# Optimization experiments

Measured on AMD Instinct MI355X. Metric: run time of the kernel, lower is better.

The kernel has to match this reference:

```python
import jax, jax.numpy as jnp
import numpy as np

TEMPERATURE = 0.1


def setup_inputs() -> dict:
    key = jax.random.key(0)
    k1, k2 = jax.random.split(key)
    N, D = 8192, 128
    features = jax.random.normal(k1, (N, D), dtype=jnp.float32)
    labels = jax.random.randint(k2, (N,), 0, 1000, dtype=jnp.int64)
    return {"features": features, "labels": labels}


def reference(features, labels):
    N = features.shape[0]
    # L2-normalize rows
    feats = features / jnp.linalg.norm(features, axis=1, keepdims=True)
    # positive-pair mask from labels [N, N]
    labels = labels.reshape(-1, 1)
    mask = (labels == labels.T).astype(feats.dtype)
    # similarity matrix scaled by temperature
    sim = jnp.matmul(feats, feats.T) / TEMPERATURE
    # exclude self-comparisons (diagonal)
    logits_mask = 1.0 - jnp.eye(N, dtype=feats.dtype)
    mask = mask * logits_mask
    exp_logits = jnp.exp(sim) * logits_mask
    log_prob = sim - jnp.log(exp_logits.sum(axis=1, keepdims=True) + 1e-9)
    mask_sum = mask.sum(axis=1)
    mask_sum = jnp.where(mask_sum == 0, jnp.ones_like(mask_sum), mask_sum)
    mean_log_prob_pos = (mask * log_prob).sum(axis=1) / mask_sum
    return -mean_log_prob_pos.mean()
```

## Files before the change

kernel.cpp:

```cpp
#include <hip/hip_runtime.h>
#include <hip/hip_bf16.h>
#include <math.h>


constexpr int N = 8192;
constexpr int D = 128;

typedef __attribute__((ext_vector_type(8))) short short8;
typedef __attribute__((ext_vector_type(4))) float f32x4;

constexpr float SELF_POISON = -50.0f;

__device__ __forceinline__ float fast_exp2(float x) {
#if __has_builtin(__builtin_amdgcn_exp2f)
    return __builtin_amdgcn_exp2f(x);
#else
    return __expf(x * 0.69314718056f);
#endif
}

__global__ void zero_kernel(int* __restrict__ hist, float* __restrict__ out) {
    hist[threadIdx.x] = 0;
    if (threadIdx.x == 0) out[0] = 0.0f;
}

__global__ void prep_kernel(const float* __restrict__ F,
                            const int* __restrict__ labels,
                            unsigned int* __restrict__ FbP,
                            int* __restrict__ hist) {
    int row = blockIdx.x * 4 + (threadIdx.x >> 6);
    int l = threadIdx.x & 63;
    float2 v = ((const float2*)(F + (size_t)row * D))[l];
    float ss = v.x * v.x + v.y * v.y;
#pragma unroll
    for (int off = 32; off > 0; off >>= 1) ss += __shfl_xor(ss, off);
    float sc = sqrtf(14.4269504089f / ss);
    __hip_bfloat16 hx = __float2bfloat16(v.x * sc);
    __hip_bfloat16 hy = __float2bfloat16(v.y * sc);
    unsigned int ux = *(unsigned short*)&hx;
    unsigned int uy = *(unsigned short*)&hy;
    unsigned int idx = ((unsigned)(row >> 4) << 10) | ((unsigned)(l >> 2) << 6) |
                       ((unsigned)(row & 15) << 2) | (unsigned)(l & 3);
    FbP[idx] = ux | (uy << 16);
    if (l == 0) atomicAdd(&hist[labels[row]], 1);
}

__global__ __launch_bounds__(256, 2) void sim_kernel(
    const short8* __restrict__ P, const int* __restrict__ labels,
    float* __restrict__ partE, float* __restrict__ partP) {
    const int ti = blockIdx.x >> 4;
    const int g  = blockIdx.x & 15;
    const int tjs = g * 4;
    const int i0 = ti * 128;

    const int t = threadIdx.x, w = t >> 6, l = t & 63;
    const int c = l & 15, quad = l >> 4;
    const int wy = w >> 1, wx = w & 1;

    short8 Af[4][4];
#pragma unroll
    for (int kk = 0; kk < 4; ++kk)
#pragma unroll
        for (int m = 0; m < 4; ++m)
            Af[kk][m] = P[(ti * 8 + wy * 4 + m) * 256 + kk * 64 + l];

    int li[4][4];
#pragma unroll
    for (int m = 0; m < 4; ++m)
#pragma unroll
        for (int r = 0; r < 4; ++r)
            li[m][r] = labels[i0 + wy * 64 + m * 16 + quad * 4 + r];

    const bool selfQuad = (quad == (c >> 2));

    float RE[4][4] = {}, RP[4][4] = {};

#pragma unroll 1
    for (int tj = tjs; tj < tjs + 4; ++tj) {
        const int j0 = tj * 128;
        int lj[4];
#pragma unroll
        for (int n = 0; n < 4; ++n) lj[n] = labels[j0 + wx * 64 + n * 16 + c];

        f32x4 acc[4][4] = {};
#pragma unroll
        for (int kk = 0; kk < 4; ++kk) {
            short8 bf[4];
#pragma unroll
            for (int n = 0; n < 4; ++n)
                bf[n] = P[(tj * 8 + wx * 4 + n) * 256 + kk * 64 + l];
#pragma unroll
            for (int m = 0; m < 4; ++m)
#pragma unroll
                for (int n = 0; n < 4; ++n)
                    acc[m][n] = __builtin_amdgcn_mfma_f32_16x16x32_bf16(
                        Af[kk][m], bf[n], acc[m][n], 0, 0, 0);
        }

        if (tj == ti && wy == wx) {
#pragma unroll
            for (int m = 0; m < 4; ++m)
#pragma unroll
                for (int r = 0; r < 4; ++r) {
                    bool cond = selfQuad && (r == (c & 3));
                    acc[m][m][r] = cond ? SELF_POISON : acc[m][m][r];
                }
        }

#pragma unroll
        for (int m = 0; m < 4; ++m) {
#pragma unroll
            for (int n = 0; n < 4; ++n) {
#pragma unroll
                for (int r = 0; r < 4; ++r) {
                    float s2 = acc[m][n][r];
                    RE[m][r] += fast_exp2(s2);
                    RP[m][r] += (li[m][r] == lj[n]) ? s2 : 0.0f;
                }
            }
        }
    }

#pragma unroll
    for (int m = 0; m < 4; ++m)
#pragma unroll
        for (int r = 0; r < 4; ++r) {
#pragma unroll
            for (int off = 1; off < 16; off <<= 1) {
                RE[m][r] += __shfl_xor(RE[m][r], off);
                RP[m][r] += __shfl_xor(RP[m][r], off);
            }
        }
    if (c == 0) {
        if (g == (ti >> 2) && wy == wx) {
#pragma unroll
            for (int m = 0; m < 4; ++m)
#pragma unroll
                for (int r = 0; r < 4; ++r) RP[m][r] -= SELF_POISON;
        }
        const int slot = g * 2 + wx;
#pragma unroll
        for (int m = 0; m < 4; ++m)
#pragma unroll
            for (int r = 0; r < 4; ++r) {
                int gi = i0 + wy * 64 + m * 16 + quad * 4 + r;
                partE[(size_t)gi * 32 + slot] = RE[m][r];
                partP[(size_t)gi * 32 + slot] = RP[m][r];
            }
    }
}

__global__ void reduce_kernel(const float* __restrict__ partE,
                              const float* __restrict__ partP,
                              const int* __restrict__ labels,
                              const int* __restrict__ hist,
                              float* __restrict__ out) {
    __shared__ float ws4[4];
    const int t = threadIdx.x, w = t >> 6, l = t & 63;
    const int half = l >> 5, sl = l & 31;
    const int rbase = blockIdx.x * 64 + w * 16;

    float a = 0.0f;
#pragma unroll
    for (int it = 0; it < 8; ++it) {
        int row = rbase + it * 2 + half;
        float se = partE[(size_t)row * 32 + sl];
        float sp = partP[(size_t)row * 32 + sl];
#pragma unroll
        for (int off = 1; off < 32; off <<= 1) {
            se += __shfl_xor(se, off);
            sp += __shfl_xor(sp, off);
        }
        if (sl == 0) {
            int cnt = hist[labels[row]] - 1;
            if (cnt > 0)
                a += logf(se + 1e-9f) - 0.69314718056f * sp / (float)cnt;
        }
    }
#pragma unroll
    for (int off = 1; off < 64; off <<= 1) a += __shfl_xor(a, off);
    if (l == 0) ws4[w] = a;
    __syncthreads();
    if (t == 0) {
        float s = ws4[0] + ws4[1] + ws4[2] + ws4[3];
        atomicAdd(out, s * (1.0f / (float)N));
    }
}

extern "C" void kernel_launch(void* const* d_in, const int* in_sizes, int n_in,
                              void* d_out, int out_size, void* d_ws, size_t ws_size,
                              hipStream_t stream) {
    const float* F      = (const float*)d_in[0];
    const int*   labels = (const int*)d_in[1];
    float* out = (float*)d_out;

    unsigned int* FbP = (unsigned int*)d_ws;
    float* partE = (float*)((char*)d_ws + (size_t)2 * 1024 * 1024);
    float* partP = partE + (size_t)N * 32;
    int*   hist  = (int*)(partP + (size_t)N * 32);

    zero_kernel<<<1, 1024, 0, stream>>>(hist, out);
    prep_kernel<<<N / 4, 256, 0, stream>>>(F, labels, FbP, hist);
    sim_kernel<<<64 * 16, 256, 0, stream>>>((const short8*)FbP, labels, partE,
                                            partP);
    reduce_kernel<<<128, 256, 0, stream>>>(partE, partP, labels, hist, out);
}
```

Measured before the change: 102.4 us.

## Exploit symmetry of similarity matrix to compute only upper-triangular tiles

The similarity matrix is symmetric, so the sim kernel now visits only tiles with tj >= ti and launches 544 blocks instead of 1024. Off-diagonal tiles also produce column-wise exp and positive-pair partial sums, which go to a new column partial buffer. The reduce kernel merges the row and column partials. This roughly halves the MFMA and exp work, at the cost of extra shuffles and stores per tile, uneven block workloads and a more complex reduction.

New measurement: 158.2 us. +54.6%, slower.

```diff
diff --git a/kernel.cpp b/kernel.cpp
--- a/kernel.cpp
+++ b/kernel.cpp
@@ -47,10 +47,14 @@
 
 __global__ __launch_bounds__(256, 2) void sim_kernel(
     const short8* __restrict__ P, const int* __restrict__ labels,
-    float* __restrict__ partE, float* __restrict__ partP) {
-    const int ti = blockIdx.x >> 4;
-    const int g  = blockIdx.x & 15;
-    const int tjs = g * 4;
+    float* __restrict__ partRowE, float* __restrict__ partRowP,
+    float* __restrict__ partColE, float* __restrict__ partColP) {
+    int bid = blockIdx.x, q = 0, base = 0;
+    while (bid >= base + 4 * (16 - q)) { base += 4 * (16 - q); ++q; }
+    int rem = bid - base, ng = 16 - q;
+    int ti = 4 * q + rem / ng;
+    int g = 15 - (rem % ng);
+    int tjs = max(ti, 4 * g), tje = 4 * g + 3;
     const int i0 = ti * 128;
 
     const int t = threadIdx.x, w = t >> 6, l = t & 63;
@@ -76,7 +80,7 @@
     float RE[4][4] = {}, RP[4][4] = {};
 
 #pragma unroll 1
-    for (int tj = tjs; tj < tjs + 4; ++tj) {
+    for (int tj = tjs; tj <= tje; ++tj) {
         const int j0 = tj * 128;
         int lj[4];
 #pragma unroll
@@ -97,25 +101,59 @@
                         Af[kk][m], bf[n], acc[m][n], 0, 0, 0);
         }
 
-        if (tj == ti && wy == wx) {
-#pragma unroll
-            for (int m = 0; m < 4; ++m)
-#pragma unroll
-                for (int r = 0; r < 4; ++r) {
-                    bool cond = selfQuad && (r == (c & 3));
-                    acc[m][m][r] = cond ? SELF_POISON : acc[m][m][r];
+        if (tj == ti) {
+            if (wy == wx) {
+#pragma unroll
+                for (int m = 0; m < 4; ++m)
+#pragma unroll
+                    for (int r = 0; r < 4; ++r) {
+                        bool cond = selfQuad && (r == (c & 3));
+                        acc[m][m][r] = cond ? SELF_POISON : acc[m][m][r];
+                    }
+            }
+#pragma unroll
+            for (int m = 0; m < 4; ++m) {
+#pragma unroll
+                for (int n = 0; n < 4; ++n) {
+#pragma unroll
+                    for (int r = 0; r < 4; ++r) {
+                        float s2 = acc[m][n][r];
+                        RE[m][r] += fast_exp2(s2);
+                        RP[m][r] += (li[m][r] == lj[n]) ? s2 : 0.0f;
+                    }
                 }
-        }
-
-#pragma unroll
-        for (int m = 0; m < 4; ++m) {
+            }
+        } else {
+            float ce[4] = {}, cp[4] = {};
+#pragma unroll
+            for (int m = 0; m < 4; ++m) {
+#pragma unroll
+                for (int n = 0; n < 4; ++n) {
+#pragma unroll
+                    for (int r = 0; r < 4; ++r) {
+                        float s2 = acc[m][n][r];
+                        float e = fast_exp2(s2);
+                        float p = (li[m][r] == lj[n]) ? s2 : 0.0f;
+                        RE[m][r] += e;
+                        RP[m][r] += p;
+                        ce[n] += e;
+                        cp[n] += p;
+                    }
+                }
+            }
 #pragma unroll
             for (int n = 0; n < 4; ++n) {
-#pragma unroll
-                for (int r = 0; r < 4; ++r) {
-                    float s2 = acc[m][n][r];
-                    RE[m][r] += fast_exp2(s2);
-                    RP[m][r] += (li[m][r] == lj[n]) ? s2 : 0.0f;
+                ce[n] += __shfl_xor(ce[n], 16);
+                ce[n] += __shfl_xor(ce[n], 32);
+                cp[n] += __shfl_xor(cp[n], 16);
+                cp[n] += __shfl_xor(cp[n], 32);
+            }
+            if (quad == 0) {
+#pragma unroll
+                for (int n = 0; n < 4; ++n) {
+                    int gj = j0 + wx * 64 + n * 16 + c;
+                    partColE[(size_t)gj * 128 + ti * 2 + wy] = ce[n];
+                    partColP[(size_t)gj * 128 + ti * 2 + wy] = cp[n];
                 }
             }
         }
@@ -144,14 +182,16 @@
 #pragma unroll
             for (int r = 0; r < 4; ++r) {
                 int gi = i0 + wy * 64 + m * 16 + quad * 4 + r;
-                partE[(size_t)gi * 32 + slot] = RE[m][r];
-                partP[(size_t)gi * 32 + slot] = RP[m][r];
-            }
-    }
-}
-
-__global__ void reduce_kernel(const float* __restrict__ partE,
-                              const float* __restrict__ partP,
+                partRowE[(size_t)gi * 32 + slot] = RE[m][r];
+                partRowP[(size_t)gi * 32 + slot] = RP[m][r];
+            }
+    }
+}
+
+__global__ void reduce_kernel(const float* __restrict__ partRowE,
+                              const float* __restrict__ partRowP,
+                              const float* __restrict__ partColE,
+                              const float* __restrict__ partColP,
                               const int* __restrict__ labels,
                               const int* __restrict__ hist,
                               float* __restrict__ out) {
@@ -164,8 +204,20 @@
 #pragma unroll
     for (int it = 0; it < 8; ++it) {
         int row = rbase + it * 2 + half;
-        float se = partE[(size_t)row * 32 + sl];
-        float sp = partP[(size_t)row * 32 + sl];
+        int tji = row >> 7, qi = tji >> 2;
+        float se = 0.0f, sp = 0.0f;
+        if (sl >= 2 * qi) {
+            se += partRowE[(size_t)row * 32 + sl];
+            sp += partRowP[(size_t)row * 32 + sl];
+        }
+#pragma unroll
+        for (int k = 0; k < 4; ++k) {
+            int idx = sl + 32 * k;
+            if (idx < 2 * tji) {
+                se += partColE[(size_t)row * 128 + idx];
+                sp += partColP[(size_t)row * 128 + idx];
+            }
+        }
 #pragma unroll
         for (int off = 1; off < 32; off <<= 1) {
             se += __shfl_xor(se, off);
@@ -194,14 +246,18 @@
     const int*   labels = (const int*)d_in[1];
     float* out = (float*)d_out;
 
-    unsigned int* FbP = (unsigned int*)d_ws;
-    float* partE = (float*)((char*)d_ws + (size_t)2 * 1024 * 1024);
-    float* partP = partE + (size_t)N * 32;
-    int*   hist  = (int*)(partP + (size_t)N * 32);
+    char* p = (char*)d_ws;
+    unsigned int* FbP = (unsigned int*)p;            p += (size_t)2 * 1024 * 1024;
+    float* partRowE = (float*)p;                     p += (size_t)N * 32 * 4;
+    float* partRowP = (float*)p;                     p += (size_t)N * 32 * 4;
+    float* partColE = (float*)p;                     p += (size_t)N * 128 * 4;
+    float* partColP = (float*)p;                     p += (size_t)N * 128 * 4;
+    int*   hist = (int*)p;
 
     zero_kernel<<<1, 1024, 0, stream>>>(hist, out);
     prep_kernel<<<N / 4, 256, 0, stream>>>(F, labels, FbP, hist);
-    sim_kernel<<<64 * 16, 256, 0, stream>>>((const short8*)FbP, labels, partE,
-                                            partP);
-    reduce_kernel<<<128, 256, 0, stream>>>(partE, partP, labels, hist, out);
-}
+    sim_kernel<<<544, 256, 0, stream>>>((const short8*)FbP, labels, partRowE,
+                                        partRowP, partColE, partColP);
+    reduce_kernel<<<128, 256, 0, stream>>>(partRowE, partRowP, partColE,
+                                           partColP, labels, hist, out);
+}
```

## Double-buffer B tiles in LDS via async global loads; compute label histogram per block

Applied to the files above, without the earlier changes.

The sim kernel now stages each 128-column B tile into a double-buffered LDS array with global_load_lds, prefetching the next tile while the current one is computed, instead of reading B fragments straight from global memory. Separately, the zero kernel and the global atomic histogram in prep are removed. Each reduce block now rebuilds the full 1024-bin label histogram in shared memory from all 8192 labels. This drops one launch and the global atomics, but adds redundant histogram work in every reduce block and extra barriers in the sim loop.

After: 97.77 us. 1.05x faster.

```diff
diff --git a/kernel.cpp b/kernel.cpp
--- a/kernel.cpp
+++ b/kernel.cpp
@@ -19,15 +19,16 @@
 #endif
 }
 
-__global__ void zero_kernel(int* __restrict__ hist, float* __restrict__ out) {
-    hist[threadIdx.x] = 0;
-    if (threadIdx.x == 0) out[0] = 0.0f;
+__device__ __forceinline__ void gload_lds16(const void* g, void* s) {
+    __builtin_amdgcn_global_load_lds(
+        (const __attribute__((address_space(1))) unsigned int*)g,
+        (__attribute__((address_space(3))) unsigned int*)s, 16, 0, 0);
 }
 
 __global__ void prep_kernel(const float* __restrict__ F,
-                            const int* __restrict__ labels,
                             unsigned int* __restrict__ FbP,
-                            int* __restrict__ hist) {
+                            float* __restrict__ out) {
+    if (blockIdx.x == 0 && threadIdx.x == 0) out[0] = 0.0f;
     int row = blockIdx.x * 4 + (threadIdx.x >> 6);
     int l = threadIdx.x & 63;
     float2 v = ((const float2*)(F + (size_t)row * D))[l];
@@ -42,12 +43,13 @@
     unsigned int idx = ((unsigned)(row >> 4) << 10) | ((unsigned)(l >> 2) << 6) |
                        ((unsigned)(row & 15) << 2) | (unsigned)(l & 3);
     FbP[idx] = ux | (uy << 16);
-    if (l == 0) atomicAdd(&hist[labels[row]], 1);
 }
 
 __global__ __launch_bounds__(256, 2) void sim_kernel(
     const short8* __restrict__ P, const int* __restrict__ labels,
     float* __restrict__ partE, float* __restrict__ partP) {
+    __shared__ short8 Bt[2][2048];
+
     const int ti = blockIdx.x >> 4;
     const int g  = blockIdx.x & 15;
     const int tjs = g * 4;
@@ -73,10 +75,21 @@
 
     const bool selfQuad = (quad == (c >> 2));
 
+#define STAGEB(BUF, TJ)                                                  \
+    _Pragma("unroll") for (int it_ = 0; it_ < 8; ++it_)                  \
+        gload_lds16(P + (size_t)(TJ) * 2048 + w * 512 + it_ * 64 + l,    \
+                    &Bt[BUF][w * 512 + it_ * 64]);
+
     float RE[4][4] = {}, RP[4][4] = {};
+
+    STAGEB(0, tjs);
+    __syncthreads();
 
 #pragma unroll 1
     for (int tj = tjs; tj < tjs + 4; ++tj) {
+        const int p = (tj - tjs) & 1;
+        if (tj < tjs + 3) STAGEB(p ^ 1, tj + 1);
+
         const int j0 = tj * 128;
         int lj[4];
 #pragma unroll
@@ -88,7 +101,7 @@
             short8 bf[4];
 #pragma unroll
             for (int n = 0; n < 4; ++n)
-                bf[n] = P[(tj * 8 + wx * 4 + n) * 256 + kk * 64 + l];
+                bf[n] = Bt[p][(wx * 4 + n) * 256 + kk * 64 + l];
 #pragma unroll
             for (int m = 0; m < 4; ++m)
 #pragma unroll
@@ -119,6 +132,8 @@
                 }
             }
         }
+
+        if (tj < tjs + 3) __syncthreads();
     }
 
 #pragma unroll
@@ -153,12 +168,19 @@
 __global__ void reduce_kernel(const float* __restrict__ partE,
                               const float* __restrict__ partP,
                               const int* __restrict__ labels,
-                              const int* __restrict__ hist,
                               float* __restrict__ out) {
+    __shared__ int hist[1024];
     __shared__ float ws4[4];
     const int t = threadIdx.x, w = t >> 6, l = t & 63;
     const int half = l >> 5, sl = l & 31;
     const int rbase = blockIdx.x * 64 + w * 16;
+
+#pragma unroll
+    for (int k = 0; k < 4; ++k) hist[t + 256 * k] = 0;
+    __syncthreads();
+#pragma unroll
+    for (int k = 0; k < 32; ++k) atomicAdd(&hist[labels[t + 256 * k]], 1);
+    __syncthreads();
 
     float a = 0.0f;
 #pragma unroll
@@ -197,11 +219,9 @@
     unsigned int* FbP = (unsigned int*)d_ws;
     float* partE = (float*)((char*)d_ws + (size_t)2 * 1024 * 1024);
     float* partP = partE + (size_t)N * 32;
-    int*   hist  = (int*)(partP + (size_t)N * 32);
-
-    zero_kernel<<<1, 1024, 0, stream>>>(hist, out);
-    prep_kernel<<<N / 4, 256, 0, stream>>>(F, labels, FbP, hist);
+
+    prep_kernel<<<N / 4, 256, 0, stream>>>(F, FbP, out);
     sim_kernel<<<64 * 16, 256, 0, stream>>>((const short8*)FbP, labels, partE,
                                             partP);
-    reduce_kernel<<<128, 256, 0, stream>>>(partE, partP, labels, hist, out);
-}
+    reduce_kernel<<<128, 256, 0, stream>>>(partE, partP, labels, out);
+}
```
